# Performance work log

Hardware: AMD Instinct MI355X
Metric: run time of the kernel (lower is better)

## Reference

```python
import jax, jax.numpy as jnp
import numpy as np

G = 2048            # number of graphs in batch
NPG = 128           # nodes per graph (fixed, implied by Linear(128*hid, 1))
IN_C = 151
HID = 64
N = G * NPG
E = 2_097_152       # intra-graph edges, avg degree 8
NEG_SLOPE = 0.2


def setup_inputs() -> dict:
    key = jax.random.key(0)
    ks = jax.random.split(key, 8)
    x = jax.random.normal(ks[0], (N, IN_C), dtype=jnp.float32)
    # intra-graph random edges: pick a graph, then src/dst within it
    g = jax.random.randint(ks[1], (E,), 0, G)
    src = g * NPG + jax.random.randint(ks[2], (E,), 0, NPG)
    dst = g * NPG + jax.random.randint(ks[3], (E,), 0, NPG)
    edge_index = jnp.stack([src, dst]).astype(jnp.int32)   # [2, E]
    W1 = jax.random.normal(ks[4], (IN_C, HID), jnp.float32) / np.sqrt(IN_C)
    att_src = jax.random.normal(ks[5], (HID,), jnp.float32) * 0.1
    att_dst = jax.random.normal(ks[6], (HID,), jnp.float32) * 0.1
    b1 = jnp.zeros((HID,), jnp.float32)
    Wlin = jax.random.normal(ks[7], (NPG * HID, 1), jnp.float32) / np.sqrt(NPG * HID)
    blin = jnp.zeros((1,), jnp.float32)
    return {"x": x, "edge_index": edge_index, "W1": W1, "att_src": att_src,
            "att_dst": att_dst, "b1": b1, "Wlin": Wlin, "blin": blin}


def gat_conv(x, edge_index, W, a_src, a_dst, b):
    """PyG GATConv, heads=1, concat=True, add_self_loops=True."""
    n = x.shape[0]
    h = x @ W                                   # [N, HID] transformed features
    loops = jnp.arange(n, dtype=edge_index.dtype)
    src = jnp.concatenate([edge_index[0], loops])
    dst = jnp.concatenate([edge_index[1], loops])
    # edge score: a_src . h[j] + a_dst . h[i], j->i
    alpha = (h @ a_src)[src] + (h @ a_dst)[dst]            # [E+N]
    alpha = jax.nn.leaky_relu(alpha, NEG_SLOPE)
    # segment softmax over incoming edges of each target node
    amax = jax.ops.segment_max(alpha, dst, num_segments=n)
    ex = jnp.exp(alpha - amax[dst])
    denom = jax.ops.segment_sum(ex, dst, num_segments=n)
    w = ex / denom[dst]                                    # [E+N]
    out = jax.ops.segment_sum(h[src] * w[:, None], dst, num_segments=n)
    return out + b


def reference(x, edge_index, W1, att_src, att_dst, b1, Wlin, blin):
    h = jax.nn.relu(gat_conv(x, edge_index, W1, att_src, att_dst, b1))  # [N, HID]
    h = h.reshape(G, NPG * HID)        # linearize(x, batch): 128 nodes/graph
    logits = h @ Wlin + blin           # [G, 1]
    return jax.nn.sigmoid(logits)
```

## Files before the change

kernel.cpp:

```cpp
#include <hip/hip_runtime.h>
#include <hip/hip_bf16.h>

#define G_ 2048
#define NPG_ 128
#define INC_ 151
#define HID_ 64
#define NNODES_ (G_ * NPG_)
#define NEDGES_ 2097152

typedef __hip_bfloat16 bf16;
typedef short bf16x8v __attribute__((ext_vector_type(8)));
typedef float f32x4 __attribute__((ext_vector_type(4)));

static __device__ __forceinline__ short f2bs(float f) {
    __hip_bfloat16 b = __float2bfloat16(f);
    return __builtin_bit_cast(short, b);
}

__global__ void __launch_bounds__(256) k0C1(const float* __restrict__ W1,
                                            bf16* __restrict__ Bt,
                                            const int* __restrict__ ei,
                                            unsigned int* __restrict__ bccount) {
    __shared__ unsigned int hist[256];
    const int tid = threadIdx.x;
    if (blockIdx.x >= 256) {
        int i = (blockIdx.x - 256) * 256 + tid;
        if (i < 64 * 160) {
            int n = i / 160, k = i - n * 160;
            float v = (k < 151) ? W1[k * 64 + n] : 0.f;
            Bt[i] = __float2bfloat16(v);
        }
        return;
    }
    hist[tid] = 0;
    __syncthreads();
    const int e0 = blockIdx.x * 8192;
    for (int e = e0 + tid; e < e0 + 8192; e += 256)
        atomicAdd(&hist[ei[e] >> 10], 1u);
    __syncthreads();
    bccount[blockIdx.x * 256 + tid] = hist[tid];
}

__global__ void __launch_bounds__(256) k1_mfma(
        const float* __restrict__ x, const bf16* __restrict__ Bt,
        const float* __restrict__ att_src, const float* __restrict__ att_dst,
        bf16* __restrict__ h, float* __restrict__ as_, float* __restrict__ ad_) {
    __shared__ __align__(16) bf16 Xs[64 * 160];
    __shared__ __align__(16) bf16 Bs[64 * 160];
    const int tid = threadIdx.x;
    const int rowbase = blockIdx.x * 64;

    {
        const uint4* bsrc = (const uint4*)Bt;
        uint4* bdst = (uint4*)Bs;
        for (int i = tid; i < 1280; i += 256) bdst[i] = bsrc[i];
    }
    for (int i = tid; i < 576; i += 256) {
        int r = i / 9, c = 151 + (i - (i / 9) * 9);
        Xs[r * 160 + c] = __float2bfloat16(0.f);
    }
    {
        const float4* xsrc = (const float4*)(x + (size_t)rowbase * 151);
        for (int i = tid; i < 2416; i += 256) {
            float4 v = xsrc[i];
            unsigned gi = 4u * (unsigned)i;
            unsigned r = gi / 151u;
            unsigned c = gi - r * 151u;
            float vv[4] = {v.x, v.y, v.z, v.w};
#pragma unroll
            for (int j = 0; j < 4; j++) {
                Xs[r * 160 + c] = __float2bfloat16(vv[j]);
                if (++c == 151u) { c = 0u; ++r; }
            }
        }
    }
    __syncthreads();

    const int wv = tid >> 6, lane = tid & 63;
    const int quad = lane >> 4, m = lane & 15;
    const int arow = wv * 16 + m;

    f32x4 acc[4];
#pragma unroll
    for (int t = 0; t < 4; t++) acc[t] = (f32x4){0.f, 0.f, 0.f, 0.f};

#pragma unroll
    for (int ks = 0; ks < 5; ks++) {
        const int k0 = ks * 32 + quad * 8;
        bf16x8v af = *(const bf16x8v*)&Xs[arow * 160 + k0];
#pragma unroll
        for (int t = 0; t < 4; t++) {
            bf16x8v bfr = *(const bf16x8v*)&Bs[(t * 16 + m) * 160 + k0];
            acc[t] = __builtin_amdgcn_mfma_f32_16x16x32_bf16(af, bfr, acc[t], 0, 0, 0);
        }
    }

    float as4[4], ad4[4];
#pragma unroll
    for (int t = 0; t < 4; t++) {
        as4[t] = att_src[t * 16 + m];
        ad4[t] = att_dst[t * 16 + m];
    }
#pragma unroll
    for (int r = 0; r < 4; r++) {
        float s = acc[0][r] * as4[0] + acc[1][r] * as4[1] +
                  acc[2][r] * as4[2] + acc[3][r] * as4[3];
        float d = acc[0][r] * ad4[0] + acc[1][r] * ad4[1] +
                  acc[2][r] * ad4[2] + acc[3][r] * ad4[3];
#pragma unroll
        for (int off = 1; off <= 8; off <<= 1) {
            s += __shfl_xor(s, off);
            d += __shfl_xor(d, off);
        }
        const int node = rowbase + wv * 16 + quad * 4 + r;
        if (m == 0) { as_[node] = s; ad_[node] = d; }
#pragma unroll
        for (int t = 0; t < 4; t++) {
            float val = acc[t][r];
            float oth = __shfl_xor(val, 1);
            if (!(lane & 1)) {
                unsigned short lo = (unsigned short)f2bs(val);
                unsigned short hi = (unsigned short)f2bs(oth);
                unsigned int u = ((unsigned int)hi << 16) | lo;
                *(unsigned int*)&h[(size_t)node * 64 + t * 16 + m] = u;
            }
        }
    }
}

__global__ void __launch_bounds__(256) kC2a(unsigned int* __restrict__ bccount,
                                            unsigned int* __restrict__ totals) {
    __shared__ unsigned int sc[256];
    const int tid = threadIdx.x, bk = blockIdx.x;
    unsigned int c = bccount[tid * 256 + bk];
    sc[tid] = c;
    __syncthreads();
    for (int off = 1; off < 256; off <<= 1) {
        unsigned int v = (tid >= off) ? sc[tid - off] : 0;
        __syncthreads();
        sc[tid] += v;
        __syncthreads();
    }
    bccount[tid * 256 + bk] = sc[tid] - c;
    if (tid == 255) totals[bk] = sc[255];
}

__global__ void __launch_bounds__(256) kC2b(const unsigned int* __restrict__ totals,
                                            unsigned int* __restrict__ cbase,
                                            unsigned int* __restrict__ base4) {
    __shared__ unsigned int sc[256];
    const int tid = threadIdx.x;
    unsigned int c = totals[tid];
    sc[tid] = c;
    __syncthreads();
    for (int off = 1; off < 256; off <<= 1) {
        unsigned int v = (tid >= off) ? sc[tid - off] : 0;
        __syncthreads();
        sc[tid] += v;
        __syncthreads();
    }
    cbase[tid] = sc[tid] - c;
    if (tid == 255) {
        cbase[256] = sc[255];
        base4[G_ * 4] = NEDGES_;
    }
}

__global__ void __launch_bounds__(256) kC3_scatter(const int* __restrict__ ei,
                                                   const unsigned int* __restrict__ bccount,
                                                   const unsigned int* __restrict__ cbase,
                                                   unsigned int* __restrict__ rbuf) {
    __shared__ unsigned int cur[256];
    const int tid = threadIdx.x;
    cur[tid] = cbase[tid] + bccount[blockIdx.x * 256 + tid];
    __syncthreads();
    const int e0 = blockIdx.x * 8192;
    for (int e = e0 + tid; e < e0 + 8192; e += 256) {
        int s = ei[e];
        int d = ei[NEDGES_ + e];
        int bk = s >> 10;
        unsigned int pos = atomicAdd(&cur[bk], 1u);
        rbuf[pos] = (((unsigned int)s & 1023u) << 7) | ((unsigned int)d & 127u);
    }
}

__global__ void __launch_bounds__(256) kC4_fine(const unsigned int* __restrict__ rbuf,
                                                const unsigned int* __restrict__ cbase,
                                                unsigned int* __restrict__ base4,
                                                unsigned short* __restrict__ eb) {
    __shared__ unsigned int lcnt[32];
    __shared__ unsigned int cur[32];
    const int tid = threadIdx.x;
    const int b = blockIdx.x;
    const unsigned int s0 = cbase[b], s1 = cbase[b + 1];
    if (tid < 32) lcnt[tid] = 0;
    __syncthreads();
    for (unsigned int i = s0 + tid; i < s1; i += 256) {
        unsigned int rec = rbuf[i];
        int key = ((rec >> 12) & 0x1C) | ((rec >> 5) & 3);
        atomicAdd(&lcnt[key], 1u);
    }
    __syncthreads();
    if (tid == 0) {
        unsigned int r = 0;
#pragma unroll
        for (int j = 0; j < 32; j++) {
            base4[b * 32 + j] = s0 + r;
            cur[j] = s0 + r;
            r += lcnt[j];
        }
    }
    __syncthreads();
    const int lane = tid & 63;
    for (unsigned int i = s0 + tid; i < s1; i += 256) {
        unsigned int rec = rbuf[i];
        int key = ((rec >> 12) & 0x1C) | ((rec >> 5) & 3);
        unsigned long long m = __ballot(1);
#pragma unroll
        for (int bit = 0; bit < 5; bit++) {
            unsigned long long bb = __ballot((key >> bit) & 1);
            m &= ((key >> bit) & 1) ? bb : ~bb;
        }
        int leader = __builtin_ctzll(m);
        int rank = __builtin_popcountll(m & ((1ull << lane) - 1ull));
        unsigned int bp = 0;
        if (lane == leader)
            bp = atomicAdd(&cur[key], (unsigned int)__builtin_popcountll(m));
        bp = __shfl((int)bp, leader);
        eb[bp + rank] = (unsigned short)(rec & 0x3FFFu);
    }
}

__global__ void __launch_bounds__(256) k3_graph(
        const unsigned short* __restrict__ eb, const unsigned int* __restrict__ base4,
        const bf16* __restrict__ h,
        const float* __restrict__ as_, const float* __restrict__ ad_,
        const float* __restrict__ b1, const float* __restrict__ Wlin,
        const float* __restrict__ blin, float* __restrict__ out) {
    __shared__ __align__(16) unsigned char lds[52736];
    short* Ab = (short*)lds;
    float* S = (float*)(lds + 34816);
    short* hT = (short*)(lds + 34816);
    float* dinv = (float*)(lds + 52224);

    const int tid = threadIdx.x;
    const int g = blockIdx.x;
    const float* asg = as_ + (g << 7);
    const float* adg = ad_ + (g << 7);
    const unsigned int* hgu = (const unsigned int*)(h + ((size_t)g << 13));

#pragma unroll 1
    for (int p = 0; p < 4; p++) {
        for (int i = tid; i < 1024; i += 256)
            ((float4*)S)[i] = make_float4(0.f, 0.f, 0.f, 0.f);
        __syncthreads();
        if (tid < 32) {
            int node = 32 * p + tid;
            float a = asg[node] + adg[node];
            a = (a > 0.f) ? a : 0.2f * a;
            atomicAdd(&S[(tid << 7) + node], __expf(a));
        }
        const unsigned int q0 = base4[(g << 2) + p];
        const unsigned int q1 = base4[(g << 2) + p + 1];
        for (unsigned int k = q0 + tid; k < q1; k += 256) {
            unsigned int v = eb[k];
            int sl = v >> 7, dl = v & 127;
            float a = asg[sl] + adg[dl];
            a = (a > 0.f) ? a : 0.2f * a;
            atomicAdd(&S[((dl & 31) << 7) + sl], __expf(a));
        }
        __syncthreads();
        float rs[2];
#pragma unroll
        for (int hf = 0; hf < 2; hf++) {
            int c = tid + (hf << 8);
            int r = c >> 4;
            int col = (c & 15) << 3;
            float4 v0 = ((const float4*)S)[c * 2];
            float4 v1 = ((const float4*)S)[c * 2 + 1];
            rs[hf] = v0.x + v0.y + v0.z + v0.w + v1.x + v1.y + v1.z + v1.w;
            bf16x8v pk = {f2bs(v0.x), f2bs(v0.y), f2bs(v0.z), f2bs(v0.w),
                          f2bs(v1.x), f2bs(v1.y), f2bs(v1.z), f2bs(v1.w)};
            *(bf16x8v*)&Ab[(32 * p + r) * 136 + col] = pk;
        }
#pragma unroll
        for (int off = 1; off <= 8; off <<= 1) {
            rs[0] += __shfl_xor(rs[0], off);
            rs[1] += __shfl_xor(rs[1], off);
        }
        if ((tid & 15) == 0) {
            dinv[32 * p + (tid >> 4)] = 1.f / rs[0];
            dinv[32 * p + 16 + (tid >> 4)] = 1.f / rs[1];
        }
        __syncthreads();
    }

    for (int idx = tid; idx < 4096; idx += 256) {
        unsigned int u = hgu[idx];
        int j = idx >> 5, f2 = idx & 31;
        hT[(2 * f2) * 136 + j] = (short)(u & 0xFFFF);
        hT[(2 * f2 + 1) * 136 + j] = (short)(u >> 16);
    }
    __syncthreads();

    const int w = tid >> 6, lane = tid & 63;
    const int quad = lane >> 4, m = lane & 15;
    const int i0 = w * 32;
    f32x4 acc[2][4];
#pragma unroll
    for (int mt = 0; mt < 2; mt++)
#pragma unroll
        for (int nt = 0; nt < 4; nt++) acc[mt][nt] = (f32x4){0.f, 0.f, 0.f, 0.f};

#pragma unroll
    for (int ks = 0; ks < 4; ks++) {
        const int k0 = ks * 32 + quad * 8;
        bf16x8v a0 = *(const bf16x8v*)&Ab[(i0 + m) * 136 + k0];
        bf16x8v a1 = *(const bf16x8v*)&Ab[(i0 + 16 + m) * 136 + k0];
#pragma unroll
        for (int nt = 0; nt < 4; nt++) {
            bf16x8v bfr = *(const bf16x8v*)&hT[(nt * 16 + m) * 136 + k0];
            acc[0][nt] = __builtin_amdgcn_mfma_f32_16x16x32_bf16(a0, bfr, acc[0][nt], 0, 0, 0);
            acc[1][nt] = __builtin_amdgcn_mfma_f32_16x16x32_bf16(a1, bfr, acc[1][nt], 0, 0, 0);
        }
    }

    float dv[2][4];
#pragma unroll
    for (int mt = 0; mt < 2; mt++)
#pragma unroll
        for (int r = 0; r < 4; r++)
            dv[mt][r] = dinv[i0 + mt * 16 + quad * 4 + r];

    float p = 0.f;
#pragma unroll
    for (int nt = 0; nt < 4; nt++) {
        float bb = b1[nt * 16 + m];
#pragma unroll
        for (int mt = 0; mt < 2; mt++) {
#pragma unroll
            for (int r = 0; r < 4; r++) {
                int il = i0 + mt * 16 + quad * 4 + r;
                float v = acc[mt][nt][r] * dv[mt][r] + bb;
                v = v > 0.f ? v : 0.f;
                p += v * Wlin[il * 64 + nt * 16 + m];
            }
        }
    }
#pragma unroll
    for (int off = 32; off; off >>= 1) p += __shfl_xor(p, off);

    __syncthreads();
    if (lane == 0) S[w] = p;
    __syncthreads();
    if (tid == 0) {
        float logit = S[0] + S[1] + S[2] + S[3] + blin[0];
        out[g] = 1.f / (1.f + __expf(-logit));
    }
}

extern "C" void kernel_launch(void* const* d_in, const int* in_sizes, int n_in,
                              void* d_out, int out_size, void* d_ws, size_t ws_size,
                              hipStream_t stream) {
    (void)in_sizes; (void)n_in; (void)out_size; (void)ws_size;
    const float* x       = (const float*)d_in[0];
    const int*   ei      = (const int*)d_in[1];
    const float* W1      = (const float*)d_in[2];
    const float* att_src = (const float*)d_in[3];
    const float* att_dst = (const float*)d_in[4];
    const float* b1      = (const float*)d_in[5];
    const float* Wlin    = (const float*)d_in[6];
    const float* blin    = (const float*)d_in[7];
    float* out = (float*)d_out;

    char* ws = (char*)d_ws;
    bf16*           h       = (bf16*)ws;
    float*          as_     = (float*)(ws + 33554432);
    float*          ad_     = (float*)(ws + 34603008);
    bf16*           Bt      = (bf16*)(ws + 35651584);
    unsigned int*   bccount = (unsigned int*)(ws + 35717120);
    unsigned int*   cbase   = (unsigned int*)(ws + 35979264);
    unsigned int*   totals  = (unsigned int*)(ws + 35983360);
    unsigned int*   base4   = (unsigned int*)(ws + 35987456);
    unsigned int*   rbuf    = (unsigned int*)(ws + 36024320);
    unsigned short* eb      = (unsigned short*)(ws + 44412928);

    k0C1<<<296, 256, 0, stream>>>(W1, Bt, ei, bccount);
    k1_mfma<<<NNODES_ / 64, 256, 0, stream>>>(x, Bt, att_src, att_dst, h, as_, ad_);
    kC2a<<<256, 256, 0, stream>>>(bccount, totals);
    kC2b<<<1, 256, 0, stream>>>(totals, cbase, base4);
    kC3_scatter<<<256, 256, 0, stream>>>(ei, bccount, cbase, rbuf);
    kC4_fine<<<256, 256, 0, stream>>>(rbuf, cbase, base4, eb);
    k3_graph<<<G_, 256, 0, stream>>>(eb, base4, h, as_, ad_, b1, Wlin, blin, out);
}
```

Baseline: 373.0 us.

## Fuse edge bucketing into one cooperative kernel and drop fine-grained sort

Merges the histogram, two prefix scans and the coarse scatter into a single cooperative kernel with grid-wide syncs, removing several launches. The per-graph, per-quarter fine sort kernel is removed. The graph kernel now scans the whole coarse bucket (eight graphs) on each of its four passes and filters records by mask. This trades a sort pass for redundant reads and branch divergence in the aggregation kernel.

```diff
diff --git a/kernel.cpp b/kernel.cpp
--- a/kernel.cpp
+++ b/kernel.cpp
@@ -1,5 +1,8 @@
 #include <hip/hip_runtime.h>
 #include <hip/hip_bf16.h>
+#include <hip/hip_cooperative_groups.h>
+
+namespace cg = cooperative_groups;
 
 #define G_ 2048
 #define NPG_ 128
@@ -17,28 +20,74 @@
     return __builtin_bit_cast(short, b);
 }
 
-__global__ void __launch_bounds__(256) k0C1(const float* __restrict__ W1,
-                                            bf16* __restrict__ Bt,
-                                            const int* __restrict__ ei,
-                                            unsigned int* __restrict__ bccount) {
-    __shared__ unsigned int hist[256];
+__global__ void __launch_bounds__(256) kSort(const int* __restrict__ ei,
+                                             const float* __restrict__ W1,
+                                             bf16* __restrict__ Bt,
+                                             unsigned int* __restrict__ bccount,
+                                             unsigned int* __restrict__ totals,
+                                             unsigned int* __restrict__ cbase,
+                                             unsigned int* __restrict__ rbuf) {
+    __shared__ unsigned int A[256];
+    __shared__ unsigned int Bb[256];
     const int tid = threadIdx.x;
-    if (blockIdx.x >= 256) {
-        int i = (blockIdx.x - 256) * 256 + tid;
-        if (i < 64 * 160) {
-            int n = i / 160, k = i - n * 160;
-            float v = (k < 151) ? W1[k * 64 + n] : 0.f;
-            Bt[i] = __float2bfloat16(v);
-        }
-        return;
-    }
-    hist[tid] = 0;
-    __syncthreads();
-    const int e0 = blockIdx.x * 8192;
+    const int bid = blockIdx.x;
+    cg::grid_group grid = cg::this_grid();
+
+    A[tid] = 0;
+    __syncthreads();
+    const int e0 = bid * 8192;
     for (int e = e0 + tid; e < e0 + 8192; e += 256)
-        atomicAdd(&hist[ei[e] >> 10], 1u);
-    __syncthreads();
-    bccount[blockIdx.x * 256 + tid] = hist[tid];
+        atomicAdd(&A[ei[e] >> 10], 1u);
+    __syncthreads();
+    bccount[bid * 256 + tid] = A[tid];
+    if (bid < 40) {
+        int i = bid * 256 + tid;
+        int n = i / 160, k = i - n * 160;
+        float v = (k < 151) ? W1[k * 64 + n] : 0.f;
+        Bt[i] = __float2bfloat16(v);
+    }
+    grid.sync();
+
+    {
+        unsigned int c = bccount[tid * 256 + bid];
+        A[tid] = c;
+        __syncthreads();
+        for (int off = 1; off < 256; off <<= 1) {
+            unsigned int v = (tid >= off) ? A[tid - off] : 0;
+            __syncthreads();
+            A[tid] += v;
+            __syncthreads();
+        }
+        bccount[tid * 256 + bid] = A[tid] - c;
+        if (tid == 255) totals[bid] = A[255];
+    }
+    grid.sync();
+
+    {
+        unsigned int c = totals[tid];
+        Bb[tid] = c;
+        __syncthreads();
+        for (int off = 1; off < 256; off <<= 1) {
+            unsigned int v = (tid >= off) ? Bb[tid - off] : 0;
+            __syncthreads();
+            Bb[tid] += v;
+            __syncthreads();
+        }
+        if (bid == 0) {
+            cbase[tid] = Bb[tid] - c;
+            if (tid == 255) cbase[256] = Bb[255];
+        }
+        A[tid] = (Bb[tid] - c) + bccount[bid * 256 + tid];
+    }
+    __syncthreads();
+
+    for (int e = e0 + tid; e < e0 + 8192; e += 256) {
+        int s = ei[e];
+        int d = ei[NEDGES_ + e];
+        int bk = s >> 10;
+        unsigned int pos = atomicAdd(&A[bk], 1u);
+        rbuf[pos] = (((unsigned int)s & 1023u) << 7) | ((unsigned int)d & 127u);
+    }
 }
 
 __global__ void __launch_bounds__(256) k1_mfma(
@@ -128,111 +177,8 @@
     }
 }
 
-__global__ void __launch_bounds__(256) kC2a(unsigned int* __restrict__ bccount,
-                                            unsigned int* __restrict__ totals) {
-    __shared__ unsigned int sc[256];
-    const int tid = threadIdx.x, bk = blockIdx.x;
-    unsigned int c = bccount[tid * 256 + bk];
-    sc[tid] = c;
-    __syncthreads();
-    for (int off = 1; off < 256; off <<= 1) {
-        unsigned int v = (tid >= off) ? sc[tid - off] : 0;
-        __syncthreads();
-        sc[tid] += v;
-        __syncthreads();
-    }
-    bccount[tid * 256 + bk] = sc[tid] - c;
-    if (tid == 255) totals[bk] = sc[255];
-}
-
-__global__ void __launch_bounds__(256) kC2b(const unsigned int* __restrict__ totals,
-                                            unsigned int* __restrict__ cbase,
-                                            unsigned int* __restrict__ base4) {
-    __shared__ unsigned int sc[256];
-    const int tid = threadIdx.x;
-    unsigned int c = totals[tid];
-    sc[tid] = c;
-    __syncthreads();
-    for (int off = 1; off < 256; off <<= 1) {
-        unsigned int v = (tid >= off) ? sc[tid - off] : 0;
-        __syncthreads();
-        sc[tid] += v;
-        __syncthreads();
-    }
-    cbase[tid] = sc[tid] - c;
-    if (tid == 255) {
-        cbase[256] = sc[255];
-        base4[G_ * 4] = NEDGES_;
-    }
-}
-
-__global__ void __launch_bounds__(256) kC3_scatter(const int* __restrict__ ei,
-                                                   const unsigned int* __restrict__ bccount,
-                                                   const unsigned int* __restrict__ cbase,
-                                                   unsigned int* __restrict__ rbuf) {
-    __shared__ unsigned int cur[256];
-    const int tid = threadIdx.x;
-    cur[tid] = cbase[tid] + bccount[blockIdx.x * 256 + tid];
-    __syncthreads();
-    const int e0 = blockIdx.x * 8192;
-    for (int e = e0 + tid; e < e0 + 8192; e += 256) {
-        int s = ei[e];
-        int d = ei[NEDGES_ + e];
-        int bk = s >> 10;
-        unsigned int pos = atomicAdd(&cur[bk], 1u);
-        rbuf[pos] = (((unsigned int)s & 1023u) << 7) | ((unsigned int)d & 127u);
-    }
-}
-
-__global__ void __launch_bounds__(256) kC4_fine(const unsigned int* __restrict__ rbuf,
-                                                const unsigned int* __restrict__ cbase,
-                                                unsigned int* __restrict__ base4,
-                                                unsigned short* __restrict__ eb) {
-    __shared__ unsigned int lcnt[32];
-    __shared__ unsigned int cur[32];
-    const int tid = threadIdx.x;
-    const int b = blockIdx.x;
-    const unsigned int s0 = cbase[b], s1 = cbase[b + 1];
-    if (tid < 32) lcnt[tid] = 0;
-    __syncthreads();
-    for (unsigned int i = s0 + tid; i < s1; i += 256) {
-        unsigned int rec = rbuf[i];
-        int key = ((rec >> 12) & 0x1C) | ((rec >> 5) & 3);
-        atomicAdd(&lcnt[key], 1u);
-    }
-    __syncthreads();
-    if (tid == 0) {
-        unsigned int r = 0;
-#pragma unroll
-        for (int j = 0; j < 32; j++) {
-            base4[b * 32 + j] = s0 + r;
-            cur[j] = s0 + r;
-            r += lcnt[j];
-        }
-    }
-    __syncthreads();
-    const int lane = tid & 63;
-    for (unsigned int i = s0 + tid; i < s1; i += 256) {
-        unsigned int rec = rbuf[i];
-        int key = ((rec >> 12) & 0x1C) | ((rec >> 5) & 3);
-        unsigned long long m = __ballot(1);
-#pragma unroll
-        for (int bit = 0; bit < 5; bit++) {
-            unsigned long long bb = __ballot((key >> bit) & 1);
-            m &= ((key >> bit) & 1) ? bb : ~bb;
-        }
-        int leader = __builtin_ctzll(m);
-        int rank = __builtin_popcountll(m & ((1ull << lane) - 1ull));
-        unsigned int bp = 0;
-        if (lane == leader)
-            bp = atomicAdd(&cur[key], (unsigned int)__builtin_popcountll(m));
-        bp = __shfl((int)bp, leader);
-        eb[bp + rank] = (unsigned short)(rec & 0x3FFFu);
-    }
-}
-
 __global__ void __launch_bounds__(256) k3_graph(
-        const unsigned short* __restrict__ eb, const unsigned int* __restrict__ base4,
+        const unsigned int* __restrict__ rbuf, const unsigned int* __restrict__ cbase,
         const bf16* __restrict__ h,
         const float* __restrict__ as_, const float* __restrict__ ad_,
         const float* __restrict__ b1, const float* __restrict__ Wlin,
@@ -249,6 +195,10 @@
     const float* adg = ad_ + (g << 7);
     const unsigned int* hgu = (const unsigned int*)(h + ((size_t)g << 13));
 
+    const unsigned int cb0 = cbase[g >> 3];
+    const unsigned int cb1 = cbase[(g >> 3) + 1];
+    const unsigned int gtag = ((unsigned int)(g & 7)) << 14;
+
 #pragma unroll 1
     for (int p = 0; p < 4; p++) {
         for (int i = tid; i < 1024; i += 256)
@@ -260,14 +210,15 @@
             a = (a > 0.f) ? a : 0.2f * a;
             atomicAdd(&S[(tid << 7) + node], __expf(a));
         }
-        const unsigned int q0 = base4[(g << 2) + p];
-        const unsigned int q1 = base4[(g << 2) + p + 1];
-        for (unsigned int k = q0 + tid; k < q1; k += 256) {
-            unsigned int v = eb[k];
-            int sl = v >> 7, dl = v & 127;
-            float a = asg[sl] + adg[dl];
-            a = (a > 0.f) ? a : 0.2f * a;
-            atomicAdd(&S[((dl & 31) << 7) + sl], __expf(a));
+        const unsigned int sel = gtag | ((unsigned int)p << 5);
+        for (unsigned int k = cb0 + tid; k < cb1; k += 256) {
+            unsigned int rec = rbuf[k];
+            if ((rec & 0x1C060u) == sel) {
+                int sl = (rec >> 7) & 127, dl = rec & 127;
+                float a = asg[sl] + adg[dl];
+                a = (a > 0.f) ? a : 0.2f * a;
+                atomicAdd(&S[((dl & 31) << 7) + sl], __expf(a));
+            }
         }
         __syncthreads();
         float rs[2];
@@ -381,15 +332,12 @@
     unsigned int*   bccount = (unsigned int*)(ws + 35717120);
     unsigned int*   cbase   = (unsigned int*)(ws + 35979264);
     unsigned int*   totals  = (unsigned int*)(ws + 35983360);
-    unsigned int*   base4   = (unsigned int*)(ws + 35987456);
-    unsigned int*   rbuf    = (unsigned int*)(ws + 36024320);
-    unsigned short* eb      = (unsigned short*)(ws + 44412928);
-
-    k0C1<<<296, 256, 0, stream>>>(W1, Bt, ei, bccount);
+    unsigned int*   rbuf    = (unsigned int*)(ws + 35987456);
+
+    void* sortArgs[] = {(void*)&ei, (void*)&W1, (void*)&Bt, (void*)&bccount,
+                        (void*)&totals, (void*)&cbase, (void*)&rbuf};
+    hipLaunchCooperativeKernel((const void*)kSort, dim3(256), dim3(256),
+                               sortArgs, 0, stream);
     k1_mfma<<<NNODES_ / 64, 256, 0, stream>>>(x, Bt, att_src, att_dst, h, as_, ad_);
-    kC2a<<<256, 256, 0, stream>>>(bccount, totals);
-    kC2b<<<1, 256, 0, stream>>>(totals, cbase, base4);
-    kC3_scatter<<<256, 256, 0, stream>>>(ei, bccount, cbase, rbuf);
-    kC4_fine<<<256, 256, 0, stream>>>(rbuf, cbase, base4, eb);
-    k3_graph<<<G_, 256, 0, stream>>>(eb, base4, h, as_, ad_, b1, Wlin, blin, out);
-}
+    k3_graph<<<G_, 256, 0, stream>>>(rbuf, cbase, h, as_, ad_, b1, Wlin, blin, out);
+}
```

Result: slower. 531.6 us (+42.5%).

## Fuse feature GEMM into per-graph kernel and split edges into finer buckets

Applied to the files above, without the earlier changes.

The separate node-feature GEMM kernel is removed. Each per-graph block now loads its 128 rows of x, computes h with MFMA directly into a transposed LDS tile, and keeps the attention scores in LDS. This drops the global round-trip of h and the attention scores and one kernel launch. The fine edge bucketing goes from 4 to 8 destination groups per graph, so each softmax pass handles 16 rows with 256 threads. The costs are more LDS per block, possibly lower occupancy, and the x load and GEMM now sit on the graph kernel's critical path with no overlap against the sort kernels.

```diff
diff --git a/kernel.cpp b/kernel.cpp
--- a/kernel.cpp
+++ b/kernel.cpp
@@ -25,8 +25,8 @@
     const int tid = threadIdx.x;
     if (blockIdx.x >= 256) {
         int i = (blockIdx.x - 256) * 256 + tid;
-        if (i < 64 * 160) {
-            int n = i / 160, k = i - n * 160;
+        if (i < 64 * 168) {
+            int n = i / 168, k = i - n * 168;
             float v = (k < 151) ? W1[k * 64 + n] : 0.f;
             Bt[i] = __float2bfloat16(v);
         }
@@ -39,93 +39,6 @@
         atomicAdd(&hist[ei[e] >> 10], 1u);
     __syncthreads();
     bccount[blockIdx.x * 256 + tid] = hist[tid];
-}
-
-__global__ void __launch_bounds__(256) k1_mfma(
-        const float* __restrict__ x, const bf16* __restrict__ Bt,
-        const float* __restrict__ att_src, const float* __restrict__ att_dst,
-        bf16* __restrict__ h, float* __restrict__ as_, float* __restrict__ ad_) {
-    __shared__ __align__(16) bf16 Xs[64 * 160];
-    __shared__ __align__(16) bf16 Bs[64 * 160];
-    const int tid = threadIdx.x;
-    const int rowbase = blockIdx.x * 64;
-
-    {
-        const uint4* bsrc = (const uint4*)Bt;
-        uint4* bdst = (uint4*)Bs;
-        for (int i = tid; i < 1280; i += 256) bdst[i] = bsrc[i];
-    }
-    for (int i = tid; i < 576; i += 256) {
-        int r = i / 9, c = 151 + (i - (i / 9) * 9);
-        Xs[r * 160 + c] = __float2bfloat16(0.f);
-    }
-    {
-        const float4* xsrc = (const float4*)(x + (size_t)rowbase * 151);
-        for (int i = tid; i < 2416; i += 256) {
-            float4 v = xsrc[i];
-            unsigned gi = 4u * (unsigned)i;
-            unsigned r = gi / 151u;
-            unsigned c = gi - r * 151u;
-            float vv[4] = {v.x, v.y, v.z, v.w};
-#pragma unroll
-            for (int j = 0; j < 4; j++) {
-                Xs[r * 160 + c] = __float2bfloat16(vv[j]);
-                if (++c == 151u) { c = 0u; ++r; }
-            }
-        }
-    }
-    __syncthreads();
-
-    const int wv = tid >> 6, lane = tid & 63;
-    const int quad = lane >> 4, m = lane & 15;
-    const int arow = wv * 16 + m;
-
-    f32x4 acc[4];
-#pragma unroll
-    for (int t = 0; t < 4; t++) acc[t] = (f32x4){0.f, 0.f, 0.f, 0.f};
-
-#pragma unroll
-    for (int ks = 0; ks < 5; ks++) {
-        const int k0 = ks * 32 + quad * 8;
-        bf16x8v af = *(const bf16x8v*)&Xs[arow * 160 + k0];
-#pragma unroll
-        for (int t = 0; t < 4; t++) {
-            bf16x8v bfr = *(const bf16x8v*)&Bs[(t * 16 + m) * 160 + k0];
-            acc[t] = __builtin_amdgcn_mfma_f32_16x16x32_bf16(af, bfr, acc[t], 0, 0, 0);
-        }
-    }
-
-    float as4[4], ad4[4];
-#pragma unroll
-    for (int t = 0; t < 4; t++) {
-        as4[t] = att_src[t * 16 + m];
-        ad4[t] = att_dst[t * 16 + m];
-    }
-#pragma unroll
-    for (int r = 0; r < 4; r++) {
-        float s = acc[0][r] * as4[0] + acc[1][r] * as4[1] +
-                  acc[2][r] * as4[2] + acc[3][r] * as4[3];
-        float d = acc[0][r] * ad4[0] + acc[1][r] * ad4[1] +
-                  acc[2][r] * ad4[2] + acc[3][r] * ad4[3];
-#pragma unroll
-        for (int off = 1; off <= 8; off <<= 1) {
-            s += __shfl_xor(s, off);
-            d += __shfl_xor(d, off);
-        }
-        const int node = rowbase + wv * 16 + quad * 4 + r;
-        if (m == 0) { as_[node] = s; ad_[node] = d; }
-#pragma unroll
-        for (int t = 0; t < 4; t++) {
-            float val = acc[t][r];
-            float oth = __shfl_xor(val, 1);
-            if (!(lane & 1)) {
-                unsigned short lo = (unsigned short)f2bs(val);
-                unsigned short hi = (unsigned short)f2bs(oth);
-                unsigned int u = ((unsigned int)hi << 16) | lo;
-                *(unsigned int*)&h[(size_t)node * 64 + t * 16 + m] = u;
-            }
-        }
-    }
 }
 
 __global__ void __launch_bounds__(256) kC2a(unsigned int* __restrict__ bccount,
@@ -147,7 +60,7 @@
 
 __global__ void __launch_bounds__(256) kC2b(const unsigned int* __restrict__ totals,
                                             unsigned int* __restrict__ cbase,
-                                            unsigned int* __restrict__ base4) {
+                                            unsigned int* __restrict__ base8) {
     __shared__ unsigned int sc[256];
     const int tid = threadIdx.x;
     unsigned int c = totals[tid];
@@ -162,7 +75,7 @@
     cbase[tid] = sc[tid] - c;
     if (tid == 255) {
         cbase[256] = sc[255];
-        base4[G_ * 4] = NEDGES_;
+        base8[G_ * 8] = NEDGES_;
     }
 }
 
@@ -186,26 +99,26 @@
 
 __global__ void __launch_bounds__(256) kC4_fine(const unsigned int* __restrict__ rbuf,
                                                 const unsigned int* __restrict__ cbase,
-                                                unsigned int* __restrict__ base4,
+                                                unsigned int* __restrict__ base8,
                                                 unsigned short* __restrict__ eb) {
-    __shared__ unsigned int lcnt[32];
-    __shared__ unsigned int cur[32];
+    __shared__ unsigned int lcnt[64];
+    __shared__ unsigned int cur[64];
     const int tid = threadIdx.x;
     const int b = blockIdx.x;
     const unsigned int s0 = cbase[b], s1 = cbase[b + 1];
-    if (tid < 32) lcnt[tid] = 0;
+    if (tid < 64) lcnt[tid] = 0;
     __syncthreads();
     for (unsigned int i = s0 + tid; i < s1; i += 256) {
         unsigned int rec = rbuf[i];
-        int key = ((rec >> 12) & 0x1C) | ((rec >> 5) & 3);
+        int key = ((rec >> 11) & 0x38) | ((rec >> 4) & 7);
         atomicAdd(&lcnt[key], 1u);
     }
     __syncthreads();
     if (tid == 0) {
         unsigned int r = 0;
 #pragma unroll
-        for (int j = 0; j < 32; j++) {
-            base4[b * 32 + j] = s0 + r;
+        for (int j = 0; j < 64; j++) {
+            base8[b * 64 + j] = s0 + r;
             cur[j] = s0 + r;
             r += lcnt[j];
         }
@@ -214,10 +127,10 @@
     const int lane = tid & 63;
     for (unsigned int i = s0 + tid; i < s1; i += 256) {
         unsigned int rec = rbuf[i];
-        int key = ((rec >> 12) & 0x1C) | ((rec >> 5) & 3);
+        int key = ((rec >> 11) & 0x38) | ((rec >> 4) & 7);
         unsigned long long m = __ballot(1);
 #pragma unroll
-        for (int bit = 0; bit < 5; bit++) {
+        for (int bit = 0; bit < 6; bit++) {
             unsigned long long bb = __ballot((key >> bit) & 1);
             m &= ((key >> bit) & 1) ? bb : ~bb;
         }
@@ -232,79 +145,137 @@
 }
 
 __global__ void __launch_bounds__(256) k3_graph(
-        const unsigned short* __restrict__ eb, const unsigned int* __restrict__ base4,
-        const bf16* __restrict__ h,
-        const float* __restrict__ as_, const float* __restrict__ ad_,
+        const float* __restrict__ x, const bf16* __restrict__ Bt,
+        const float* __restrict__ att_src, const float* __restrict__ att_dst,
+        const unsigned short* __restrict__ eb, const unsigned int* __restrict__ base8,
         const float* __restrict__ b1, const float* __restrict__ Wlin,
         const float* __restrict__ blin, float* __restrict__ out) {
-    __shared__ __align__(16) unsigned char lds[52736];
+    __shared__ __align__(16) unsigned char lds[61952];
+    short* Bs = (short*)lds;
+    short* Xs = (short*)(lds + 21504);
     short* Ab = (short*)lds;
     float* S = (float*)(lds + 34816);
-    short* hT = (short*)(lds + 34816);
-    float* dinv = (float*)(lds + 52224);
+    short* hT = (short*)(lds + 43008);
+    float* asL = (float*)(lds + 60416);
+    float* adL = (float*)(lds + 60928);
+    float* dinv = (float*)(lds + 61440);
 
     const int tid = threadIdx.x;
     const int g = blockIdx.x;
-    const float* asg = as_ + (g << 7);
-    const float* adg = ad_ + (g << 7);
-    const unsigned int* hgu = (const unsigned int*)(h + ((size_t)g << 13));
+    const int w = tid >> 6, lane = tid & 63;
+    const int quad = lane >> 4, m = lane & 15;
+
+    {
+        const uint4* bsrc = (const uint4*)Bt;
+        uint4* bdst = (uint4*)Bs;
+        for (int i = tid; i < 1344; i += 256) bdst[i] = bsrc[i];
+    }
+    float as4[4], ad4[4];
+#pragma unroll
+    for (int t = 0; t < 4; t++) {
+        as4[t] = att_src[t * 16 + m];
+        ad4[t] = att_dst[t * 16 + m];
+    }
 
 #pragma unroll 1
-    for (int p = 0; p < 4; p++) {
-        for (int i = tid; i < 1024; i += 256)
+    for (int half = 0; half < 2; half++) {
+        for (int i = tid; i < 576; i += 256) {
+            int r = i / 9, c = 151 + (i - (i / 9) * 9);
+            Xs[r * 168 + c] = 0;
+        }
+        const float4* xsrc = (const float4*)(x + ((size_t)g * 128 + half * 64) * 151);
+        for (int i = tid; i < 2416; i += 256) {
+            float4 v = xsrc[i];
+            unsigned gi = 4u * (unsigned)i;
+            unsigned r = gi / 151u;
+            unsigned c = gi - r * 151u;
+            float vv[4] = {v.x, v.y, v.z, v.w};
+#pragma unroll
+            for (int j = 0; j < 4; j++) {
+                Xs[r * 168 + c] = f2bs(vv[j]);
+                if (++c == 151u) { c = 0u; ++r; }
+            }
+        }
+        __syncthreads();
+
+        f32x4 acc[4];
+#pragma unroll
+        for (int t = 0; t < 4; t++) acc[t] = (f32x4){0.f, 0.f, 0.f, 0.f};
+        const int xrow = w * 16 + m;
+#pragma unroll
+        for (int ks = 0; ks < 5; ks++) {
+            const int k0 = ks * 32 + quad * 8;
+            bf16x8v af = *(const bf16x8v*)&Xs[xrow * 168 + k0];
+#pragma unroll
+            for (int t = 0; t < 4; t++) {
+                bf16x8v bfr = *(const bf16x8v*)&Bs[(t * 16 + m) * 168 + k0];
+                acc[t] = __builtin_amdgcn_mfma_f32_16x16x32_bf16(af, bfr, acc[t], 0, 0, 0);
+            }
+        }
+        const int node0 = half * 64 + w * 16 + quad * 4;
+#pragma unroll
+        for (int r = 0; r < 4; r++) {
+            float s = acc[0][r] * as4[0] + acc[1][r] * as4[1] +
+                      acc[2][r] * as4[2] + acc[3][r] * as4[3];
+            float d = acc[0][r] * ad4[0] + acc[1][r] * ad4[1] +
+                      acc[2][r] * ad4[2] + acc[3][r] * ad4[3];
+#pragma unroll
+            for (int off = 1; off <= 8; off <<= 1) {
+                s += __shfl_xor(s, off);
+                d += __shfl_xor(d, off);
+            }
+            if (m == 0) { asL[node0 + r] = s; adL[node0 + r] = d; }
+        }
+#pragma unroll
+        for (int t = 0; t < 4; t++) {
+            const int col = t * 16 + m;
+            unsigned int u01 = ((unsigned int)(unsigned short)f2bs(acc[t][1]) << 16) |
+                               (unsigned short)f2bs(acc[t][0]);
+            unsigned int u23 = ((unsigned int)(unsigned short)f2bs(acc[t][3]) << 16) |
+                               (unsigned short)f2bs(acc[t][2]);
+            *(unsigned int*)&hT[col * 136 + node0] = u01;
+            *(unsigned int*)&hT[col * 136 + node0 + 2] = u23;
+        }
+        __syncthreads();
+    }
+
+#pragma unroll 1
+    for (int p = 0; p < 8; p++) {
+        for (int i = tid; i < 512; i += 256)
             ((float4*)S)[i] = make_float4(0.f, 0.f, 0.f, 0.f);
         __syncthreads();
-        if (tid < 32) {
-            int node = 32 * p + tid;
-            float a = asg[node] + adg[node];
+        if (tid < 16) {
+            int node = 16 * p + tid;
+            float a = asL[node] + adL[node];
             a = (a > 0.f) ? a : 0.2f * a;
             atomicAdd(&S[(tid << 7) + node], __expf(a));
         }
-        const unsigned int q0 = base4[(g << 2) + p];
-        const unsigned int q1 = base4[(g << 2) + p + 1];
+        const unsigned int q0 = base8[(g << 3) + p];
+        const unsigned int q1 = base8[(g << 3) + p + 1];
         for (unsigned int k = q0 + tid; k < q1; k += 256) {
             unsigned int v = eb[k];
             int sl = v >> 7, dl = v & 127;
-            float a = asg[sl] + adg[dl];
+            float a = asL[sl] + adL[dl];
             a = (a > 0.f) ? a : 0.2f * a;
-            atomicAdd(&S[((dl & 31) << 7) + sl], __expf(a));
-        }
-        __syncthreads();
-        float rs[2];
-#pragma unroll
-        for (int hf = 0; hf < 2; hf++) {
-            int c = tid + (hf << 8);
-            int r = c >> 4;
-            int col = (c & 15) << 3;
-            float4 v0 = ((const float4*)S)[c * 2];
-            float4 v1 = ((const float4*)S)[c * 2 + 1];
-            rs[hf] = v0.x + v0.y + v0.z + v0.w + v1.x + v1.y + v1.z + v1.w;
+            atomicAdd(&S[((dl & 15) << 7) + sl], __expf(a));
+        }
+        __syncthreads();
+        {
+            int r = tid >> 4;
+            int col = (tid & 15) << 3;
+            float4 v0 = ((const float4*)S)[tid * 2];
+            float4 v1 = ((const float4*)S)[tid * 2 + 1];
+            float rs = v0.x + v0.y + v0.z + v0.w + v1.x + v1.y + v1.z + v1.w;
             bf16x8v pk = {f2bs(v0.x), f2bs(v0.y), f2bs(v0.z), f2bs(v0.w),
                           f2bs(v1.x), f2bs(v1.y), f2bs(v1.z), f2bs(v1.w)};
-            *(bf16x8v*)&Ab[(32 * p + r) * 136 + col] = pk;
-        }
-#pragma unroll
-        for (int off = 1; off <= 8; off <<= 1) {
-            rs[0] += __shfl_xor(rs[0], off);
-            rs[1] += __shfl_xor(rs[1], off);
-        }
-        if ((tid & 15) == 0) {
-            dinv[32 * p + (tid >> 4)] = 1.f / rs[0];
-            dinv[32 * p + 16 + (tid >> 4)] = 1.f / rs[1];
-        }
-        __syncthreads();
-    }
-
-    for (int idx = tid; idx < 4096; idx += 256) {
-        unsigned int u = hgu[idx];
-        int j = idx >> 5, f2 = idx & 31;
-        hT[(2 * f2) * 136 + j] = (short)(u & 0xFFFF);
-        hT[(2 * f2 + 1) * 136 + j] = (short)(u >> 16);
-    }
-    __syncthreads();
-
-    const int w = tid >> 6, lane = tid & 63;
-    const int quad = lane >> 4, m = lane & 15;
+            *(bf16x8v*)&Ab[(16 * p + r) * 136 + col] = pk;
+#pragma unroll
+            for (int off = 1; off <= 8; off <<= 1) rs += __shfl_xor(rs, off);
+            if ((tid & 15) == 0) dinv[16 * p + r] = 1.f / rs;
+        }
+        __syncthreads();
+    }
+
     const int i0 = w * 32;
     f32x4 acc[2][4];
 #pragma unroll
@@ -332,7 +303,7 @@
         for (int r = 0; r < 4; r++)
             dv[mt][r] = dinv[i0 + mt * 16 + quad * 4 + r];
 
-    float p = 0.f;
+    float pacc = 0.f;
 #pragma unroll
     for (int nt = 0; nt < 4; nt++) {
         float bb = b1[nt * 16 + m];
@@ -343,15 +314,15 @@
                 int il = i0 + mt * 16 + quad * 4 + r;
                 float v = acc[mt][nt][r] * dv[mt][r] + bb;
                 v = v > 0.f ? v : 0.f;
-                p += v * Wlin[il * 64 + nt * 16 + m];
+                pacc += v * Wlin[il * 64 + nt * 16 + m];
             }
         }
     }
 #pragma unroll
-    for (int off = 32; off; off >>= 1) p += __shfl_xor(p, off);
-
-    __syncthreads();
-    if (lane == 0) S[w] = p;
+    for (int off = 32; off; off >>= 1) pacc += __shfl_xor(pacc, off);
+
+    __syncthreads();
+    if (lane == 0) S[w] = pacc;
     __syncthreads();
     if (tid == 0) {
         float logit = S[0] + S[1] + S[2] + S[3] + blin[0];
@@ -374,22 +345,19 @@
     float* out = (float*)d_out;
 
     char* ws = (char*)d_ws;
-    bf16*           h       = (bf16*)ws;
-    float*          as_     = (float*)(ws + 33554432);
-    float*          ad_     = (float*)(ws + 34603008);
-    bf16*           Bt      = (bf16*)(ws + 35651584);
-    unsigned int*   bccount = (unsigned int*)(ws + 35717120);
-    unsigned int*   cbase   = (unsigned int*)(ws + 35979264);
-    unsigned int*   totals  = (unsigned int*)(ws + 35983360);
-    unsigned int*   base4   = (unsigned int*)(ws + 35987456);
-    unsigned int*   rbuf    = (unsigned int*)(ws + 36024320);
-    unsigned short* eb      = (unsigned short*)(ws + 44412928);
-
-    k0C1<<<296, 256, 0, stream>>>(W1, Bt, ei, bccount);
-    k1_mfma<<<NNODES_ / 64, 256, 0, stream>>>(x, Bt, att_src, att_dst, h, as_, ad_);
+    bf16*           Bt      = (bf16*)ws;
+    unsigned int*   bccount = (unsigned int*)(ws + 65536);
+    unsigned int*   cbase   = (unsigned int*)(ws + 327680);
+    unsigned int*   totals  = (unsigned int*)(ws + 331776);
+    unsigned int*   base8   = (unsigned int*)(ws + 335872);
+    unsigned int*   rbuf    = (unsigned int*)(ws + 405504);
+    unsigned short* eb      = (unsigned short*)(ws + 8794112);
+
+    k0C1<<<298, 256, 0, stream>>>(W1, Bt, ei, bccount);
     kC2a<<<256, 256, 0, stream>>>(bccount, totals);
-    kC2b<<<1, 256, 0, stream>>>(totals, cbase, base4);
+    kC2b<<<1, 256, 0, stream>>>(totals, cbase, base8);
     kC3_scatter<<<256, 256, 0, stream>>>(ei, bccount, cbase, rbuf);
-    kC4_fine<<<256, 256, 0, stream>>>(rbuf, cbase, base4, eb);
-    k3_graph<<<G_, 256, 0, stream>>>(eb, base4, h, as_, ad_, b1, Wlin, blin, out);
-}
+    kC4_fine<<<256, 256, 0, stream>>>(rbuf, cbase, base8, eb);
+    k3_graph<<<G_, 256, 0, stream>>>(x, Bt, att_src, att_dst, eb, base8,
+                                     b1, Wlin, blin, out);
+}
```

Measured after the change: 381.2 us. +2.2%, slower.
